# Optimization experiments

Measured on AMD Instinct MI355X. Metric: run time of the kernel, lower is better.

Reference implementation:

```python
import jax, jax.numpy as jnp
import numpy as np

B, L = 128, 1024
V, E, H = 32, 256, 1024


def setup_inputs() -> dict:
    key = jax.random.key(0)
    ks = jax.random.split(key, 6)
    return {
        "x": jax.random.randint(ks[0], (B, L), 0, V),
        "hidden": jnp.zeros((B, H), dtype=jnp.float32),
        "embedding": jax.random.normal(ks[1], (V, E), dtype=jnp.float32),
        "W_e": jax.random.normal(ks[2], (E, H), dtype=jnp.float32) * 0.01,
        "W_h": jax.random.normal(ks[3], (H, H), dtype=jnp.float32) * 0.01,
        "b_h": jnp.zeros((H,), dtype=jnp.float32),
        "W_o": jax.random.normal(ks[4], (H, V), dtype=jnp.float32) * 0.01,
        "b_o": jnp.zeros((V,), dtype=jnp.float32),
    }


def reference(x, hidden, embedding, W_e, W_h, b_h, W_o, b_o):
    # x: [B, L] int -> embed: [B, L, E]
    x_embed = embedding[x]
    # Precompute the input projection for all timesteps at once: [L, B, H]
    xin = jnp.einsum("ble,eh->lbh", x_embed, W_e) + b_h

    def step(h, x_t):
        # h: [B, H], x_t: [B, H] (already projected + bias)
        h_new = jnp.tanh(x_t + h @ W_h)
        return h_new, h_new

    final_hidden, outputs = jax.lax.scan(step, hidden, xin)
    # outputs: [L, B, H] -> [B, L, H]
    outputs = outputs.transpose(1, 0, 2)
    logits = outputs @ W_o + b_o  # [B, L, V]
    return logits, final_hidden
```

## Files before the change

### kernel.cpp

```cpp
#include <hip/hip_runtime.h>

typedef unsigned short u16;
typedef unsigned int   u32;
typedef __attribute__((ext_vector_type(4))) float floatx4;
typedef __attribute__((ext_vector_type(4))) u32  u32x4;
typedef __attribute__((ext_vector_type(8))) short short8;

#define B_SZ  128
#define L_SEQ 1024
#define V_SZ  32
#define E_SZ  256
#define H_SZ  1024

#define N_GROUPS     8
#define WG_PER_GROUP 8
#define N_BLOCKS     (N_GROUPS * WG_PER_GROUP)
#define LOGIT_BASE   (B_SZ * L_SEQ * V_SZ)

#define BAR_BYTES  8192
#define FLAG_OFF   (BAR_BYTES - 8)
#define P_OFF      BAR_BYTES
#define P_BYTES    (V_SZ * H_SZ * 4)
#define HBUF_OFF   (P_OFF + P_BYTES)
#define NBUF       4
#define HBUF_G     (NBUF * 16 * H_SZ)
#define HBUF_BYTES (N_GROUPS * HBUF_G * 2)

#define SENT 0xFFFFFFFFu

#define MFMA16x16x32(a, b, c) __builtin_amdgcn_mfma_f32_16x16x32_bf16(a, b, c, 0, 0, 0)

__device__ inline float b2f(u16 u) {
    union { unsigned i; float f; } x; x.i = ((unsigned)u) << 16; return x.f;
}
__device__ inline u16 f2b(float f) {
    unsigned u = __float_as_uint(f);
    return (u16)((u + 0x7FFFu + ((u >> 16) & 1u)) >> 16);
}
__device__ inline float ldf(const void* p, long i, int isf32) {
    return isf32 ? ((const float*)p)[i] : b2f(((const u16*)p)[i]);
}
__device__ inline u16 ldb(const void* p, long i, int isf32) {
    return isf32 ? f2b(((const float*)p)[i]) : ((const u16*)p)[i];
}

__device__ inline float fast_tanh(float x) {
    float cx = fminf(fmaxf(x, -15.f), 15.f);
    float t  = __builtin_amdgcn_exp2f(cx * 2.885390081777927f);
    return (t - 1.f) * __builtin_amdgcn_rcpf(t + 1.f);
}

__device__ inline void ld_row16_raw(const u16* abase, u32x4 a[8]) {
    u32x4 a0, a1, a2, a3, a4, a5, a6, a7;
    asm volatile(
        "global_load_dwordx4 %0, %8, off offset:0   sc0 sc1\n\t"
        "global_load_dwordx4 %1, %8, off offset:64  sc0 sc1\n\t"
        "global_load_dwordx4 %2, %8, off offset:128 sc0 sc1\n\t"
        "global_load_dwordx4 %3, %8, off offset:192 sc0 sc1\n\t"
        "global_load_dwordx4 %4, %8, off offset:256 sc0 sc1\n\t"
        "global_load_dwordx4 %5, %8, off offset:320 sc0 sc1\n\t"
        "global_load_dwordx4 %6, %8, off offset:384 sc0 sc1\n\t"
        "global_load_dwordx4 %7, %8, off offset:448 sc0 sc1\n\t"
        "s_waitcnt vmcnt(0)"
        : "=&v"(a0), "=&v"(a1), "=&v"(a2), "=&v"(a3),
          "=&v"(a4), "=&v"(a5), "=&v"(a6), "=&v"(a7)
        : "v"(abase)
        : "memory");
    a[0] = a0; a[1] = a1; a[2] = a2; a[3] = a3;
    a[4] = a4; a[5] = a5; a[6] = a6; a[7] = a7;
}
__device__ inline u32 maxdw4(u32x4 a) {
    u32 m0 = a[0] > a[1] ? a[0] : a[1];
    u32 m1 = a[2] > a[3] ? a[2] : a[3];
    return m0 > m1 ? m0 : m1;
}
__device__ inline int row_ok(const u32x4 a[8]) {
    u32 m = maxdw4(a[0]);
    #pragma unroll
    for (int j = 1; j < 8; ++j) { u32 t = maxdw4(a[j]); m = t > m ? t : m; }
    return (int)(m != SENT);
}
__device__ inline void poll_row16(const u16* abase, short8 afr[8]) {
    u32x4 av[8];
    ld_row16_raw(abase, av);
    long guard = 0;
    while (!__all(row_ok(av))) {
        if (++guard > 100000L) break;
        ld_row16_raw(abase, av);
    }
    union { u32x4 v; short8 s; } u;
    #pragma unroll
    for (int j = 0; j < 8; ++j) { u.v = av[j]; afr[j] = u.s; }
}
__device__ inline void st_row16(u32* p, u32x4 d) {
    asm volatile("global_store_dwordx4 %0, %1, off sc0 sc1" :: "v"(p), "v"(d) : "memory");
}

__global__ void detect_dtype(const u16* __restrict__ emb, const int* __restrict__ xi,
                             int* __restrict__ flag) {
    float v = b2f(emb[threadIdx.x]);
    if (!(fabsf(v) <= 1.0e6f)) atomicOr(flag, 1);
    if (xi[2 * threadIdx.x + 1] != 0) atomicOr(flag, 2);
}

__global__ void precompute_P(const void* __restrict__ emb, const void* __restrict__ We,
                             const void* __restrict__ bh, float* __restrict__ P,
                             const int* __restrict__ flag) {
    const int isf32 = *flag & 1;
    int o = blockIdx.x * 256 + threadIdx.x;
    int v = o >> 10, h = o & (H_SZ - 1);
    float acc = ldf(bh, h, isf32);
    for (int e = 0; e < E_SZ; ++e)
        acc += ldf(emb, v * E_SZ + e, isf32) * ldf(We, (long)e * H_SZ + h, isf32);
    P[o] = acc;
}

__global__ void __launch_bounds__(256, 1) rnn_kernel(
    const void* __restrict__ xp, const void* __restrict__ hidden,
    const void* __restrict__ Wh, const void* __restrict__ Wo,
    const void* __restrict__ bo, const float* __restrict__ P,
    u16* __restrict__ hbuf, float* __restrict__ out,
    const int* __restrict__ flag)
{
    __shared__ __align__(16) float red[12800];

    const int fl    = *flag;
    const int isf32 = fl & 1;
    const int xi64  = !(fl & 2);
    const int g     = blockIdx.x & 7;
    const int wg    = blockIdx.x >> 3;
    const int col0  = wg * 128;
    const int b0    = g * 16;
    const int tid   = threadIdx.x;
    const int wave  = tid >> 6;
    const int lane  = tid & 63;
    const int lrow  = lane & 15;
    const int quad  = lane >> 4;
    const int kwave = wave * 256;

    const int* x32       = (const int*)xp;
    const long long* x64 = (const long long*)xp;

    u16* hb = hbuf + g * HBUF_G;

    short8 whf[8][8], wof[2][8];
    #pragma unroll
    for (int kk = 0; kk < 8; ++kk) {
        const int kb = kwave + kk * 32 + quad * 8;
        #pragma unroll
        for (int j = 0; j < 8; ++j) {
            #pragma unroll
            for (int nt = 0; nt < 8; ++nt)
                whf[nt][kk][j] = (short)ldb(Wh, (long)(kb + j) * H_SZ + col0 + nt * 16 + lrow, isf32);
            wof[0][kk][j] = (short)ldb(Wo, (long)(kb + j) * V_SZ + lrow, isf32);
            wof[1][kk][j] = (short)ldb(Wo, (long)(kb + j) * V_SZ + 16 + lrow, isf32);
        }
    }

    const int bq = tid >> 4;
    const int c0 = (tid & 15) * 8;
    const float bov0 = ldf(bo, (tid & 15) * 2, isf32);
    const float bov1 = ldf(bo, (tid & 15) * 2 + 1, isf32);

    {
        u32x4 d;
        #pragma unroll
        for (int p = 0; p < 4; ++p) {
            u16 lo = ldb(hidden, (long)(b0 + bq) * H_SZ + col0 + c0 + 2 * p, isf32);
            u16 hi = ldb(hidden, (long)(b0 + bq) * H_SZ + col0 + c0 + 2 * p + 1, isf32);
            d[p] = (u32)lo | ((u32)hi << 16);
        }
        st_row16((u32*)(hb + bq * H_SZ + col0 + c0), d);
    }

    for (int s = 0; s < L_SEQ; ++s) {
        const u16* hc = hb + (s & 3) * (16 * H_SZ);
        u16* hn       = hb + ((s + 1) & 3) * (16 * H_SZ);
        u16* hcl      = hb + ((s + 3) & 3) * (16 * H_SZ);
        const bool do_logit = (wg == (s & 7));

        long xoff = (long)(b0 + bq) * L_SEQ + s;
        int xv = xi64 ? (int)x64[xoff] : x32[xoff];
        const floatx4* pp = (const floatx4*)(P + (long)xv * H_SZ + col0 + c0);
        floatx4 pv0 = pp[0], pv1 = pp[1];

        short8 afr[8];
        poll_row16(hc + lrow * H_SZ + kwave + quad * 8, afr);

        floatx4 acc[8] = {};
        #pragma unroll
        for (int kk = 0; kk < 8; ++kk)
            #pragma unroll
            for (int nt = 0; nt < 8; ++nt)
                acc[nt] = MFMA16x16x32(afr[kk], whf[nt][kk], acc[nt]);
        if (do_logit) {
            floatx4 aL0 = {0,0,0,0}, aL1 = {0,0,0,0};
            #pragma unroll
            for (int kk = 0; kk < 8; ++kk) {
                aL0 = MFMA16x16x32(afr[kk], wof[0][kk], aL0);
                aL1 = MFMA16x16x32(afr[kk], wof[1][kk], aL1);
            }
            #pragma unroll
            for (int r = 0; r < 4; ++r) {
                red[10240 + wave * 640 +       (quad * 4 + r) * 20 + lrow] = aL0[r];
                red[10240 + wave * 640 + 320 + (quad * 4 + r) * 20 + lrow] = aL1[r];
            }
        }

        #pragma unroll
        for (int nt = 0; nt < 8; ++nt)
            #pragma unroll
            for (int r = 0; r < 4; ++r)
                red[wave * 2560 + nt * 320 + (quad * 4 + r) * 20 + lrow] = acc[nt][r];
        __syncthreads();

        {
            const int base = (c0 >> 4) * 320 + bq * 20 + (c0 & 15);
            floatx4 s0 = {0,0,0,0}, s1 = {0,0,0,0};
            #pragma unroll
            for (int w = 0; w < 4; ++w) {
                s0 += *(const floatx4*)&red[w * 2560 + base];
                s1 += *(const floatx4*)&red[w * 2560 + base + 4];
            }
            float h[8];
            #pragma unroll
            for (int j = 0; j < 4; ++j) h[j]     = fast_tanh(s0[j] + pv0[j]);
            #pragma unroll
            for (int j = 0; j < 4; ++j) h[4 + j] = fast_tanh(s1[j] + pv1[j]);
            u32x4 d;
            #pragma unroll
            for (int p = 0; p < 4; ++p)
                d[p] = (u32)f2b(h[2 * p]) | ((u32)f2b(h[2 * p + 1]) << 16);
            st_row16((u32*)(hn + bq * H_SZ + col0 + c0), d);
            if (s == L_SEQ - 1) {
                float* op = out + LOGIT_BASE + (long)(b0 + bq) * H_SZ + col0 + c0;
                ((floatx4*)op)[0] = floatx4{h[0], h[1], h[2], h[3]};
                ((floatx4*)op)[1] = floatx4{h[4], h[5], h[6], h[7]};
            }
        }
        {
            u32x4 f = { SENT, SENT, SENT, SENT };
            st_row16((u32*)(hcl + bq * H_SZ + col0 + c0), f);
        }

        if (do_logit && s >= 1) {
            int v0 = (tid & 15) * 2;
            int lb = 10240 + (v0 >> 4) * 320 + bq * 20 + (v0 & 15);
            float q0 = 0.f, q1 = 0.f;
            #pragma unroll
            for (int w = 0; w < 4; ++w) {
                q0 += red[lb + w * 640];
                q1 += red[lb + w * 640 + 1];
            }
            long ob = ((long)(b0 + bq) * L_SEQ + (s - 1)) * V_SZ + v0;
            out[ob]     = q0 + bov0;
            out[ob + 1] = q1 + bov1;
        }
        __syncthreads();
    }

    if (wg == 0) {
        short8 afr[8];
        poll_row16(hb + lrow * H_SZ + kwave + quad * 8, afr);
        floatx4 aL0 = {0,0,0,0}, aL1 = {0,0,0,0};
        #pragma unroll
        for (int kk = 0; kk < 8; ++kk) {
            aL0 = MFMA16x16x32(afr[kk], wof[0][kk], aL0);
            aL1 = MFMA16x16x32(afr[kk], wof[1][kk], aL1);
        }
        #pragma unroll
        for (int r = 0; r < 4; ++r) {
            red[10240 + wave * 640 +       (quad * 4 + r) * 20 + lrow] = aL0[r];
            red[10240 + wave * 640 + 320 + (quad * 4 + r) * 20 + lrow] = aL1[r];
        }
        __syncthreads();
        {
            int v0 = (tid & 15) * 2;
            int lb = 10240 + (v0 >> 4) * 320 + bq * 20 + (v0 & 15);
            float q0 = 0.f, q1 = 0.f;
            #pragma unroll
            for (int w = 0; w < 4; ++w) {
                q0 += red[lb + w * 640];
                q1 += red[lb + w * 640 + 1];
            }
            long ob = ((long)(b0 + bq) * L_SEQ + (L_SEQ - 1)) * V_SZ + v0;
            out[ob]     = q0 + bov0;
            out[ob + 1] = q1 + bov1;
        }
    }
}

extern "C" void kernel_launch(void* const* d_in, const int* in_sizes, int n_in,
                              void* d_out, int out_size, void* d_ws, size_t ws_size,
                              hipStream_t stream) {
    (void)in_sizes; (void)n_in; (void)out_size; (void)ws_size;
    const void* x      = d_in[0];
    const void* hidden = d_in[1];
    const void* emb    = d_in[2];
    const void* We     = d_in[3];
    const void* Wh     = d_in[4];
    const void* bh     = d_in[5];
    const void* Wo     = d_in[6];
    const void* bo     = d_in[7];
    float* out = (float*)d_out;

    char* ws = (char*)d_ws;
    int*   flag = (int*)(ws + FLAG_OFF);
    float* P    = (float*)(ws + P_OFF);
    u16*   hbuf = (u16*)(ws + HBUF_OFF);

    hipMemsetAsync(ws, 0, BAR_BYTES, stream);
    hipMemsetAsync(ws + HBUF_OFF, 0xFF, HBUF_BYTES, stream);

    detect_dtype<<<dim3(1), dim3(256), 0, stream>>>((const u16*)emb, (const int*)x, flag);
    precompute_P<<<dim3(128), dim3(256), 0, stream>>>(emb, We, bh, P, flag);

    rnn_kernel<<<dim3(N_BLOCKS), dim3(256), 0, stream>>>(
        x, hidden, Wh, Wo, bo, P, hbuf, out, flag);
}
```

Measured before the change: 3.225 ms.

## Prefetch next-step input projection and poll with lightweight probe loads

The token index and the projected-input row for step s+1 are now loaded during step s, so their global-memory latency overlaps the MFMA work instead of sitting on the recurrent critical path. The readiness poll first spins on two cheap dword loads before issuing the full row load, which reduces memory traffic while waiting on other workgroups. Sentinel clearing is skipped for the last two steps. The prefetch adds register pressure, and the probe only checks two dwords, so the full-row check is still needed for correctness.

```diff
diff --git a/kernel.cpp b/kernel.cpp
--- a/kernel.cpp
+++ b/kernel.cpp
@@ -82,8 +82,20 @@
 }
 __device__ inline void poll_row16(const u16* abase, short8 afr[8]) {
     u32x4 av[8];
+    long guard = 0;
+    {
+        u32 p0, p1;
+        for (;;) {
+            asm volatile(
+                "global_load_dword %0, %2, off sc0 sc1\n\t"
+                "global_load_dword %1, %2, off offset:256 sc0 sc1\n\t"
+                "s_waitcnt vmcnt(0)"
+                : "=&v"(p0), "=&v"(p1) : "v"(abase) : "memory");
+            if (__all((int)((p0 != SENT) & (p1 != SENT)))) break;
+            if (++guard > 100000L) break;
+        }
+    }
     ld_row16_raw(abase, av);
-    long guard = 0;
     while (!__all(row_ok(av))) {
         if (++guard > 100000L) break;
         ld_row16_raw(abase, av);
@@ -173,19 +185,27 @@
         st_row16((u32*)(hb + bq * H_SZ + col0 + c0), d);
     }
 
+    int xv = xi64 ? (int)x64[(long)(b0 + bq) * L_SEQ] : x32[(long)(b0 + bq) * L_SEQ];
+    floatx4 pv0, pv1;
+    {
+        const floatx4* pp = (const floatx4*)(P + (long)xv * H_SZ + col0 + c0);
+        pv0 = pp[0]; pv1 = pp[1];
+    }
+
     for (int s = 0; s < L_SEQ; ++s) {
         const u16* hc = hb + (s & 3) * (16 * H_SZ);
         u16* hn       = hb + ((s + 1) & 3) * (16 * H_SZ);
         u16* hcl      = hb + ((s + 3) & 3) * (16 * H_SZ);
         const bool do_logit = (wg == (s & 7));
 
-        long xoff = (long)(b0 + bq) * L_SEQ + s;
-        int xv = xi64 ? (int)x64[xoff] : x32[xoff];
-        const floatx4* pp = (const floatx4*)(P + (long)xv * H_SZ + col0 + c0);
-        floatx4 pv0 = pp[0], pv1 = pp[1];
-
         short8 afr[8];
         poll_row16(hc + lrow * H_SZ + kwave + quad * 8, afr);
+
+        int xn = 0;
+        if (s + 1 < L_SEQ) {
+            long xo = (long)(b0 + bq) * L_SEQ + s + 1;
+            xn = xi64 ? (int)x64[xo] : x32[xo];
+        }
 
         floatx4 acc[8] = {};
         #pragma unroll
@@ -205,6 +225,12 @@
                 red[10240 + wave * 640 +       (quad * 4 + r) * 20 + lrow] = aL0[r];
                 red[10240 + wave * 640 + 320 + (quad * 4 + r) * 20 + lrow] = aL1[r];
             }
+        }
+
+        floatx4 pvn0, pvn1;
+        {
+            const floatx4* ppn = (const floatx4*)(P + (long)xn * H_SZ + col0 + c0);
+            pvn0 = ppn[0]; pvn1 = ppn[1];
         }
 
         #pragma unroll
@@ -238,7 +264,7 @@
                 ((floatx4*)op)[1] = floatx4{h[4], h[5], h[6], h[7]};
             }
         }
-        {
+        if (s <= L_SEQ - 3) {
             u32x4 f = { SENT, SENT, SENT, SENT };
             st_row16((u32*)(hcl + bq * H_SZ + col0 + c0), f);
         }
@@ -257,6 +283,8 @@
             out[ob + 1] = q1 + bov1;
         }
         __syncthreads();
+
+        xv = xn; pv0 = pvn0; pv1 = pvn1;
     }
 
     if (wg == 0) {
```

Measured after the change: 3.729 ms. 15.6% more time.
